# Kernel tuning notes

Measured on AMD Instinct MI355X. Metric: run time of the kernel, lower is better.

## Reference

```python
import jax, jax.numpy as jnp
import numpy as np
import hashlib

MAX_HASH_VALUE = 2 ** 8  # 256
BATCH, MAX_LEN, EMB, HID, VOCAB = 32, 512, 256, 1024, 32000


def _hash_mod(flat_ids, algo):
    # SHA digest interpreted little-endian; only value mod 256 matters for the
    # downstream (h1 + k*h2) % 256, and mod 256 of a little-endian int is just
    # the first digest byte. We keep the full int.from_bytes for faithfulness.
    return np.array(
        [int.from_bytes(algo(str(int(v)).encode()).digest(), 'little') % MAX_HASH_VALUE
         for v in flat_ids],
        dtype=np.int64,
    )


def setup_inputs() -> dict:
    key = jax.random.key(0)
    k1, k2, k3 = jax.random.split(key, 3)
    input_ids = jax.random.randint(k1, (BATCH, MAX_LEN), 0, VOCAB, dtype=jnp.int64)
    W = jax.random.normal(k2, (HID, EMB), dtype=jnp.float32) * (1.0 / np.sqrt(EMB))
    b = jax.random.normal(k3, (HID,), dtype=jnp.float32) * 0.01
    return {"input_ids": input_ids, "W": W, "b": b}


def reference(input_ids, W, b):
    ids = np.asarray(input_ids)            # [B, L] int
    B, L = ids.shape
    flat = ids.reshape(-1)
    h1 = _hash_mod(flat, hashlib.sha256).reshape(B, L)   # [B, L] in [0,256)
    h2 = _hash_mod(flat, hashlib.sha224).reshape(B, L)
    k = jnp.arange(EMB, dtype=jnp.int64)                 # [E]
    # hash3[b,l,k] = (h1 + k*h2) % 256
    hash3 = ((jnp.asarray(h1)[:, :, None] + k[None, None, :] * jnp.asarray(h2)[:, :, None])
             % MAX_HASH_VALUE).astype(jnp.float32)        # [B, L, E]
    out = jnp.einsum('ble,he->blh', hash3, W) + b        # [B, L, H]
    return out
```

## Files before the change

### kernel.cpp

```cpp
#include <hip/hip_runtime.h>
#include <stdint.h>

typedef short bf16x8 __attribute__((ext_vector_type(8)));
typedef float f32x16 __attribute__((ext_vector_type(16)));
typedef float f32x4 __attribute__((ext_vector_type(4)));
typedef unsigned short ushort_t;

#define EMB 256
#define HID 1024
#define NTOK 16384

#define WS_W_OFF 0

#define ROTR(x,n) (((x)>>(n))|((x)<<(32-(n))))
#define S0F(x) (ROTR((x),7)^ROTR((x),18)^((x)>>3))
#define S1F(x) (ROTR((x),17)^ROTR((x),19)^((x)>>10))

#define RND1(Kc, Wt) do {                                                          \
    uint32_t t1_ = sh + (ROTR(se,6)^ROTR(se,11)^ROTR(se,25))                       \
                   + ((se&sf)^(~se&sg)) + (Kc) + (Wt);                             \
    uint32_t t2_ = (ROTR(sa,2)^ROTR(sa,13)^ROTR(sa,22))                            \
                   + ((sa&sb)^(sa&sc)^(sb&sc));                                    \
    sh=sg; sg=sf; sf=se; se=sd+t1_; sd=sc; sc=sb; sb=sa; sa=t1_+t2_; } while (0)

#define WSXS(a,b,c,d) ((a) += S0F(b) + (c) + S1F(d))

__device__ __forceinline__ uint32_t rbf(float x) {
    uint32_t b = __float_as_uint(x);
    return (b + 0x7FFFu + ((b >> 16) & 1u)) >> 16;
}
__device__ __forceinline__ uint4 pack8(float4 a, float4 b) {
    uint4 q;
    q.x = rbf(a.x) | (rbf(a.y) << 16);
    q.y = rbf(a.z) | (rbf(a.w) << 16);
    q.z = rbf(b.x) | (rbf(b.y) << 16);
    q.w = rbf(b.z) | (rbf(b.w) << 16);
    return q;
}

#define MFMA(av,bv,acc) __builtin_amdgcn_mfma_f32_32x32x16_bf16(av,bv,acc,0,0,0)

__global__ __launch_bounds__(64) void prep_kernel(const float* __restrict__ W,
                                                  ushort_t* __restrict__ Wf) {
    const int t = (int)blockIdx.x * 64 + (int)threadIdx.x;
    const int h = t >> 4;
    const int kk = t & 15;
    const float4* wsrc = reinterpret_cast<const float4*>(W + h * EMB + kk * 16);
    float4 a = wsrc[0], b = wsrc[1], c = wsrc[2], d = wsrc[3];
    const int P = h >> 7, hl = h & 127, j = hl & 3, cc = hl >> 2;
    uint4* wbase = reinterpret_cast<uint4*>(Wf)
                   + ((size_t)(P * 4 + j) * 16 + kk) * 64 + cc;
    wbase[0]  = pack8(a, b);
    wbase[32] = pack8(c, d);
}

__global__ __launch_bounds__(256, 2) void fused_kernel(const uint32_t* __restrict__ ids32,
                                                       const ushort_t* __restrict__ Wf,
                                                       const float* __restrict__ bias,
                                                       float* __restrict__ out) {
    __shared__ uint4 Albuf[4096];
    __shared__ uint32_t redf[4];

    const int bid = blockIdx.x;
    const int bm = bid >> 2;
    const int nb0 = (bid & 3) * 256;
    const int tid = (int)threadIdx.x;
    const int wv = tid >> 6, lane = tid & 63, lrow = lane & 31, lh = lane >> 5;
    const int wm = wv >> 1;
    const int wn2 = wv & 1;

    {
        const uint4* ids4 = reinterpret_cast<const uint4*>(ids32);
        uint4 da = ids4[tid], db = ids4[tid + 256];
        uint32_t z = da.y | da.w | db.y | db.w;
        unsigned long long m = __ballot(z != 0u);
        if (lane == 0) redf[wv] = (m != 0ull) ? 1u : 0u;
    }
    __syncthreads();
    const bool is64 = (redf[0] | redf[1] | redf[2] | redf[3]) == 0u;

    const int rr = tid >> 1;
    const uint32_t st = tid & 1;
    const int tok = bm * 128 + rr;
    const uint32_t v = is64 ? ids32[2 * tok] : ids32[tok];

    const uint32_t q4 = __umulhi(v, 0xD1B71759u) >> 13;
    const uint32_t r4 = v - q4 * 10000u;
    const uint32_t q3 = __umulhi(r4, 0x10624DD3u) >> 6;
    const uint32_t r3 = r4 - q3 * 1000u;
    const uint32_t q2 = __umulhi(r3, 0x51EB851Fu) >> 5;
    const uint32_t r2 = r3 - q2 * 100u;
    const uint32_t q1 = __umulhi(r2, 0xCCCCCCCDu) >> 3;
    const uint32_t q0 = r2 - q1 * 10u;
    const uint32_t nd = v >= 10000u ? 5u : v >= 1000u ? 4u : v >= 100u ? 3u
                         : v >= 10u ? 2u : 1u;
    uint64_t M = ((uint64_t)(q4 + '0') << 56) | ((uint64_t)(q3 + '0') << 48) |
                 ((uint64_t)(q2 + '0') << 40) | ((uint64_t)(q1 + '0') << 32) |
                 ((uint64_t)(q0 + '0') << 24) | ((uint64_t)0x80u << 16);
    M <<= 8u * (5u - nd);

    uint32_t w0 = (uint32_t)(M >> 32), w1 = (uint32_t)M;
    uint32_t w2 = 0, w3 = 0, w4 = 0, w5 = 0, w6 = 0, w7 = 0;
    uint32_t w8 = 0, w9 = 0, w10 = 0, w11 = 0, w12 = 0, w13 = 0, w14 = 0;
    uint32_t w15 = nd * 8u;

    uint32_t sa = st ? 0xc1059ed8u : 0x6a09e667u;
    uint32_t sb = st ? 0x367cd507u : 0xbb67ae85u;
    uint32_t sc = st ? 0x3070dd17u : 0x3c6ef372u;
    uint32_t sd = st ? 0xf70e5939u : 0xa54ff53au;
    uint32_t se = st ? 0xffc00b31u : 0x510e527fu;
    uint32_t sf = st ? 0x68581511u : 0x9b05688cu;
    uint32_t sg = st ? 0x64f98fa7u : 0x1f83d9abu;
    uint32_t sh = st ? 0xbefa4fa4u : 0x5be0cd19u;

    RND1(0x428a2f98u, w0);  RND1(0x71374491u, w1);  RND1(0xb5c0fbcfu, w2);
    RND1(0xe9b5dba5u, w3);  RND1(0x3956c25bu, w4);  RND1(0x59f111f1u, w5);
    RND1(0x923f82a4u, w6);  RND1(0xab1c5ed5u, w7);  RND1(0xd807aa98u, w8);
    RND1(0x12835b01u, w9);  RND1(0x243185beu, w10); RND1(0x550c7dc3u, w11);
    RND1(0x72be5d74u, w12); RND1(0x80deb1feu, w13); RND1(0x9bdc06a7u, w14);
    RND1(0xc19bf174u, w15);
    WSXS(w0,w1,w9,w14);    RND1(0xe49b69c1u, w0);
    WSXS(w1,w2,w10,w15);   RND1(0xefbe4786u, w1);
    WSXS(w2,w3,w11,w0);    RND1(0x0fc19dc6u, w2);
    WSXS(w3,w4,w12,w1);    RND1(0x240ca1ccu, w3);
    WSXS(w4,w5,w13,w2);    RND1(0x2de92c6fu, w4);
    WSXS(w5,w6,w14,w3);    RND1(0x4a7484aau, w5);
    WSXS(w6,w7,w15,w4);    RND1(0x5cb0a9dcu, w6);
    WSXS(w7,w8,w0,w5);     RND1(0x76f988dau, w7);
    WSXS(w8,w9,w1,w6);     RND1(0x983e5152u, w8);
    WSXS(w9,w10,w2,w7);    RND1(0xa831c66du, w9);
    WSXS(w10,w11,w3,w8);   RND1(0xb00327c8u, w10);
    WSXS(w11,w12,w4,w9);   RND1(0xbf597fc7u, w11);
    WSXS(w12,w13,w5,w10);  RND1(0xc6e00bf3u, w12);
    WSXS(w13,w14,w6,w11);  RND1(0xd5a79147u, w13);
    WSXS(w14,w15,w7,w12);  RND1(0x06ca6351u, w14);
    WSXS(w15,w0,w8,w13);   RND1(0x14292967u, w15);
    WSXS(w0,w1,w9,w14);    RND1(0x27b70a85u, w0);
    WSXS(w1,w2,w10,w15);   RND1(0x2e1b2138u, w1);
    WSXS(w2,w3,w11,w0);    RND1(0x4d2c6dfcu, w2);
    WSXS(w3,w4,w12,w1);    RND1(0x53380d13u, w3);
    WSXS(w4,w5,w13,w2);    RND1(0x650a7354u, w4);
    WSXS(w5,w6,w14,w3);    RND1(0x766a0abbu, w5);
    WSXS(w6,w7,w15,w4);    RND1(0x81c2c92eu, w6);
    WSXS(w7,w8,w0,w5);     RND1(0x92722c85u, w7);
    WSXS(w8,w9,w1,w6);     RND1(0xa2bfe8a1u, w8);
    WSXS(w9,w10,w2,w7);    RND1(0xa81a664bu, w9);
    WSXS(w10,w11,w3,w8);   RND1(0xc24b8b70u, w10);
    WSXS(w11,w12,w4,w9);   RND1(0xc76c51a3u, w11);
    WSXS(w12,w13,w5,w10);  RND1(0xd192e819u, w12);
    WSXS(w13,w14,w6,w11);  RND1(0xd6990624u, w13);
    WSXS(w14,w15,w7,w12);  RND1(0xf40e3585u, w14);
    WSXS(w15,w0,w8,w13);   RND1(0x106aa070u, w15);
    WSXS(w0,w1,w9,w14);    RND1(0x19a4c116u, w0);
    WSXS(w1,w2,w10,w15);   RND1(0x1e376c08u, w1);
    WSXS(w2,w3,w11,w0);    RND1(0x2748774cu, w2);
    WSXS(w3,w4,w12,w1);    RND1(0x34b0bcb5u, w3);
    WSXS(w4,w5,w13,w2);    RND1(0x391c0cb3u, w4);
    WSXS(w5,w6,w14,w3);    RND1(0x4ed8aa4au, w5);
    WSXS(w6,w7,w15,w4);    RND1(0x5b9cca4fu, w6);
    WSXS(w7,w8,w0,w5);     RND1(0x682e6ff3u, w7);
    WSXS(w8,w9,w1,w6);     RND1(0x748f82eeu, w8);
    WSXS(w9,w10,w2,w7);    RND1(0x78a5636fu, w9);
    WSXS(w10,w11,w3,w8);   RND1(0x84c87814u, w10);
    WSXS(w11,w12,w4,w9);   RND1(0x8cc70208u, w11);
    WSXS(w12,w13,w5,w10);  RND1(0x90befffau, w12);
    WSXS(w13,w14,w6,w11);  RND1(0xa4506cebu, w13);
    WSXS(w14,w15,w7,w12);  RND1(0xbef9a3f7u, w14);
    WSXS(w15,w0,w8,w13);   RND1(0xc67178f2u, w15);

    const uint32_t hv = ((st ? 0xc1059ed8u : 0x6a09e667u) + sa) >> 24;
    const uint32_t hvo = __shfl_xor(hv, 1);
    const uint32_t hv1 = st ? hvo : hv;
    const uint32_t hv2 = st ? hv : hvo;

    {
        const int ag = rr >> 5, aslot = rr & 31;
        uint32_t val = (hv1 + (st ? ((hv2 << 7) & 255u) : 0u)) & 255u;
        const int kfb = (int)st * 8;
#define PAIR(dst) { uint32_t lo_ = val; uint32_t hi_ = (val + hv2) & 255u;        \
                    val = (hi_ + hv2) & 255u;                                     \
                    dst = (__float_as_uint((float)lo_) >> 16) |                   \
                          (__float_as_uint((float)hi_) & 0xFFFF0000u); }
#pragma unroll
        for (int q = 0; q < 8; ++q) {
            uint32_t c0_, c1_, c2_, c3_, c4_, c5_, c6_, c7_;
            PAIR(c0_); PAIR(c1_); PAIR(c2_); PAIR(c3_);
            PAIR(c4_); PAIR(c5_); PAIR(c6_); PAIR(c7_);
            uint4 qa; qa.x = c0_; qa.y = c1_; qa.z = c2_; qa.w = c3_;
            uint4 qb; qb.x = c4_; qb.y = c5_; qb.z = c6_; qb.w = c7_;
            Albuf[(ag * 16 + kfb + q) * 64 + aslot]      = qa;
            Albuf[(ag * 16 + kfb + q) * 64 + aslot + 32] = qb;
        }
#undef PAIR
    }

    const int C0 = nb0 + wn2 * 128;
    const f32x4 b4 = *reinterpret_cast<const f32x4*>(bias + C0 + 4 * lrow);

    __syncthreads();

    const bf16x8* bfr = reinterpret_cast<const bf16x8*>(Wf);
    const bf16x8* alr = reinterpret_cast<const bf16x8*>(Albuf);
    const int gb0 = (C0 >> 7) * 4;
    const int agA0 = (wm * 2) * 16, agA1 = (wm * 2 + 1) * 16;

    f32x16 A00 = (f32x16)(0.0f), A01 = (f32x16)(0.0f);
    f32x16 A02 = (f32x16)(0.0f), A03 = (f32x16)(0.0f);
    f32x16 A10 = (f32x16)(0.0f), A11 = (f32x16)(0.0f);
    f32x16 A12 = (f32x16)(0.0f), A13 = (f32x16)(0.0f);

#pragma unroll 2
    for (int kf = 0; kf < 16; ++kf) {
        bf16x8 av0 = alr[(agA0 + kf) * 64 + lane];
        bf16x8 av1 = alr[(agA1 + kf) * 64 + lane];
        bf16x8 bv0 = bfr[((size_t)((gb0 + 0) * 16 + kf)) * 64 + lane];
        bf16x8 bv1 = bfr[((size_t)((gb0 + 1) * 16 + kf)) * 64 + lane];
        bf16x8 bv2 = bfr[((size_t)((gb0 + 2) * 16 + kf)) * 64 + lane];
        bf16x8 bv3 = bfr[((size_t)((gb0 + 3) * 16 + kf)) * 64 + lane];
        A00 = MFMA(av0, bv0, A00); A01 = MFMA(av0, bv1, A01);
        A02 = MFMA(av0, bv2, A02); A03 = MFMA(av0, bv3, A03);
        A10 = MFMA(av1, bv0, A10); A11 = MFMA(av1, bv1, A11);
        A12 = MFMA(av1, bv2, A12); A13 = MFMA(av1, bv3, A13);
    }

    const int m0 = bm * 128 + wm * 64;
    float* obase = out + (size_t)C0 + 4 * lrow;
#pragma unroll
    for (int r = 0; r < 16; ++r) {
        const int rowl = (r & 3) + 8 * (r >> 2) + 4 * lh;
        f32x4 v0, v1;
        v0[0] = A00[r] + b4[0]; v0[1] = A01[r] + b4[1];
        v0[2] = A02[r] + b4[2]; v0[3] = A03[r] + b4[3];
        v1[0] = A10[r] + b4[0]; v1[1] = A11[r] + b4[1];
        v1[2] = A12[r] + b4[2]; v1[3] = A13[r] + b4[3];
        __builtin_nontemporal_store(
            v0, reinterpret_cast<f32x4*>(obase + (size_t)(m0 + rowl) * HID));
        __builtin_nontemporal_store(
            v1, reinterpret_cast<f32x4*>(obase + (size_t)(m0 + 32 + rowl) * HID));
    }
}

extern "C" void kernel_launch(void* const* d_in, const int* in_sizes, int n_in,
                              void* d_out, int out_size, void* d_ws, size_t ws_size,
                              hipStream_t stream) {
    const uint32_t* ids32 = (const uint32_t*)d_in[0];
    const float* W = (const float*)d_in[1];
    const float* bias = (const float*)d_in[2];
    float* out = (float*)d_out;
    ushort_t* Wf = (ushort_t*)((char*)d_ws + WS_W_OFF);
    (void)in_sizes; (void)n_in; (void)out_size; (void)ws_size;

    prep_kernel<<<256, 64, 0, stream>>>(W, Wf);
    fused_kernel<<<512, 256, 0, stream>>>(ids32, Wf, bias, out);
}
```

Before: 35.32 us.

## Hoist per-token SHA hashing into prep kernel to avoid redundant recomputation

```diff
diff --git a/kernel.cpp b/kernel.cpp
--- a/kernel.cpp
+++ b/kernel.cpp
@@ -11,6 +11,7 @@
 #define NTOK 16384
 
 #define WS_W_OFF 0
+#define WS_H_OFF (512u * 1024u)
 
 #define ROTR(x,n) (((x)>>(n))|((x)<<(32-(n))))
 #define S0F(x) (ROTR((x),7)^ROTR((x),18)^((x)>>3))
@@ -40,48 +41,30 @@
 
 #define MFMA(av,bv,acc) __builtin_amdgcn_mfma_f32_32x32x16_bf16(av,bv,acc,0,0,0)
 
-__global__ __launch_bounds__(64) void prep_kernel(const float* __restrict__ W,
-                                                  ushort_t* __restrict__ Wf) {
-    const int t = (int)blockIdx.x * 64 + (int)threadIdx.x;
-    const int h = t >> 4;
-    const int kk = t & 15;
-    const float4* wsrc = reinterpret_cast<const float4*>(W + h * EMB + kk * 16);
-    float4 a = wsrc[0], b = wsrc[1], c = wsrc[2], d = wsrc[3];
-    const int P = h >> 7, hl = h & 127, j = hl & 3, cc = hl >> 2;
-    uint4* wbase = reinterpret_cast<uint4*>(Wf)
-                   + ((size_t)(P * 4 + j) * 16 + kk) * 64 + cc;
-    wbase[0]  = pack8(a, b);
-    wbase[32] = pack8(c, d);
-}
-
-__global__ __launch_bounds__(256, 2) void fused_kernel(const uint32_t* __restrict__ ids32,
-                                                       const ushort_t* __restrict__ Wf,
-                                                       const float* __restrict__ bias,
-                                                       float* __restrict__ out) {
-    __shared__ uint4 Albuf[4096];
-    __shared__ uint32_t redf[4];
-
-    const int bid = blockIdx.x;
-    const int bm = bid >> 2;
-    const int nb0 = (bid & 3) * 256;
+__global__ __launch_bounds__(128) void prep_kernel(const uint32_t* __restrict__ ids32,
+                                                   const float* __restrict__ W,
+                                                   ushort_t* __restrict__ Wf,
+                                                   ushort_t* __restrict__ Hs) {
+    __shared__ uint32_t redf[2];
     const int tid = (int)threadIdx.x;
-    const int wv = tid >> 6, lane = tid & 63, lrow = lane & 31, lh = lane >> 5;
-    const int wm = wv >> 1;
-    const int wn2 = wv & 1;
+    const int g = (int)blockIdx.x * 128 + tid;
+
+    const int h = g >> 5, c8 = g & 31, kk = c8 >> 1, h8 = c8 & 1;
+    const float4* wsrc = reinterpret_cast<const float4*>(W + h * EMB + kk * 16 + h8 * 8);
+    float4 wa = wsrc[0], wb = wsrc[1];
 
     {
         const uint4* ids4 = reinterpret_cast<const uint4*>(ids32);
-        uint4 da = ids4[tid], db = ids4[tid + 256];
+        uint4 da = ids4[tid], db = ids4[tid + 128];
         uint32_t z = da.y | da.w | db.y | db.w;
         unsigned long long m = __ballot(z != 0u);
-        if (lane == 0) redf[wv] = (m != 0ull) ? 1u : 0u;
+        if ((tid & 63) == 0) redf[tid >> 6] = (m != 0ull) ? 1u : 0u;
     }
     __syncthreads();
-    const bool is64 = (redf[0] | redf[1] | redf[2] | redf[3]) == 0u;
-
-    const int rr = tid >> 1;
-    const uint32_t st = tid & 1;
-    const int tok = bm * 128 + rr;
+    const bool is64 = (redf[0] | redf[1]) == 0u;
+
+    const int tok = g >> 1;
+    const uint32_t st = g & 1;
     const uint32_t v = is64 ? ids32[2 * tok] : ids32[tok];
 
     const uint32_t q4 = __umulhi(v, 0xD1B71759u) >> 13;
@@ -170,10 +153,33 @@
 
     const uint32_t hv = ((st ? 0xc1059ed8u : 0x6a09e667u) + sa) >> 24;
     const uint32_t hvo = __shfl_xor(hv, 1);
-    const uint32_t hv1 = st ? hvo : hv;
-    const uint32_t hv2 = st ? hv : hvo;
+    if (st == 0) Hs[tok] = (ushort_t)(hv | (hvo << 8));
+
+    const int P = h >> 7, hl = h & 127, j = hl & 3, cc = hl >> 2;
+    uint4* wbase = reinterpret_cast<uint4*>(Wf)
+                   + ((size_t)(P * 4 + j) * 16 + kk) * 64 + cc + h8 * 32;
+    *wbase = pack8(wa, wb);
+}
+
+__global__ __launch_bounds__(256, 2) void fused_kernel(const ushort_t* __restrict__ Hs,
+                                                       const ushort_t* __restrict__ Wf,
+                                                       const float* __restrict__ bias,
+                                                       float* __restrict__ out) {
+    __shared__ uint4 Albuf[4096];
+
+    const int bid = blockIdx.x;
+    const int bm = bid >> 2;
+    const int nb0 = (bid & 3) * 256;
+    const int tid = (int)threadIdx.x;
+    const int wv = tid >> 6, lane = tid & 63, lrow = lane & 31, lh = lane >> 5;
+    const int wm = wv >> 1;
+    const int wn2 = wv & 1;
 
     {
+        const int rr = tid >> 1;
+        const uint32_t st = tid & 1;
+        const uint32_t hsv = Hs[bm * 128 + rr];
+        const uint32_t hv1 = hsv & 255u, hv2 = hsv >> 8;
         const int ag = rr >> 5, aslot = rr & 31;
         uint32_t val = (hv1 + (st ? ((hv2 << 7) & 255u) : 0u)) & 255u;
         const int kfb = (int)st * 8;
@@ -248,8 +254,9 @@
     const float* bias = (const float*)d_in[2];
     float* out = (float*)d_out;
     ushort_t* Wf = (ushort_t*)((char*)d_ws + WS_W_OFF);
+    ushort_t* Hs = (ushort_t*)((char*)d_ws + WS_H_OFF);
     (void)in_sizes; (void)n_in; (void)out_size; (void)ws_size;
 
-    prep_kernel<<<256, 64, 0, stream>>>(W, Wf);
-    fused_kernel<<<512, 256, 0, stream>>>(ids32, Wf, bias, out);
-}
+    prep_kernel<<<256, 128, 0, stream>>>(ids32, W, Wf, Hs);
+    fused_kernel<<<512, 256, 0, stream>>>(Hs, Wf, bias, out);
+}
```

Measured after the change: 32.92 us. 6.8% less time.
